# Performance work log

Measured on AMD Instinct MI355X. Metric: run time of the kernel, lower is better.

The kernel has to match this reference:

```python
import jax, jax.numpy as jnp
import numpy as np

ALPHA = 0.9  # init alpha, adj='DAD'


def setup_inputs() -> dict:
    key = jax.random.key(0)
    k1, k2, k3, k4 = jax.random.split(key, 4)
    N, C, E = 100000, 64, 3200000
    labels = jax.random.uniform(k1, (N, C), dtype=jnp.float32)
    mask = jax.random.randint(k2, (N,), 0, 2).astype(bool)
    src = jax.random.randint(k3, (E,), 0, N, dtype=jnp.int64)
    dst = jax.random.randint(k4, (E,), 0, N, dtype=jnp.int64)
    return {"labels": labels, "mask": mask, "src": src, "dst": dst, "num_layers": 10}


def reference(labels, mask, src, dst, num_layers):
    N = labels.shape[0]
    # mask: y = zeros; y[mask] = labels[mask]
    y0 = jnp.where(mask[:, None], labels, jnp.zeros((), labels.dtype))
    last = (1.0 - ALPHA) * y0  # confidence = 1
    # in-degrees via scatter-count at dst, clamped to >= 1
    degs = jax.ops.segment_sum(jnp.ones(dst.shape, labels.dtype), dst, num_segments=N)
    degs = jnp.maximum(degs, 1.0)
    norm = (degs ** -0.5)[:, None]  # DAD: D^-1/2 on both sides

    def step(y, _):
        y = norm * y                                   # left D^-1/2
        h = jax.ops.segment_sum(y[src], dst, num_segments=N)  # A @ y (copy_u + sum)
        y = ALPHA * h * norm                           # right D^-1/2
        y = jnp.clip(last + y, 0.0, 1.0)               # post_step clamp
        return y, None

    y, _ = jax.lax.scan(step, y0, None, length=num_layers)
    return y
```

## Files before the change

### kernel.cpp

```cpp
#include <hip/hip_runtime.h>
#include <hip/hip_fp16.h>


#define ALPHA 0.9f
#define C 64
#define BSHIFT 9
#define NCHUNK 256

typedef float f32x4 __attribute__((ext_vector_type(4)));
typedef unsigned int u32;


__global__ void chunk_hist_kernel(const int* __restrict__ dst, int* __restrict__ cnt,
                                  int E, int epc) {
    __shared__ int h[256];
    h[threadIdx.x] = 0;
    __syncthreads();
    int c = blockIdx.x;
    int e1 = min(c * epc + epc, E);
    for (int e = c * epc + threadIdx.x; e < e1; e += 256) {
        int d = __builtin_nontemporal_load(&dst[e]);
        atomicAdd(&h[d >> BSHIFT], 1);
    }
    __syncthreads();
    cnt[c * 256 + threadIdx.x] = h[threadIdx.x];
}

__global__ void bucket_scan_kernel(int* __restrict__ cnt, int* __restrict__ bucket_base,
                                   int* __restrict__ row_ptr, int N, int E) {
    __shared__ int tmp[256];
    int b = threadIdx.x;
    int s = 0;
    for (int c = 0; c < NCHUNK; ++c) {
        int t = cnt[c * 256 + b];
        cnt[c * 256 + b] = s;
        s += t;
    }
    tmp[b] = s;
    __syncthreads();
    int v = s;
    for (int off = 1; off < 256; off <<= 1) {
        int add = (b >= off) ? tmp[b - off] : 0;
        __syncthreads();
        tmp[b] += add;
        __syncthreads();
    }
    bucket_base[b] = tmp[b] - v;
    if (b == 255) { bucket_base[256] = tmp[255]; row_ptr[N] = E; }
}

__global__ void bucket_scatter_kernel(const int* __restrict__ src, const int* __restrict__ dst,
                                      const int* __restrict__ cnt,
                                      const int* __restrict__ bucket_base,
                                      unsigned* __restrict__ tmp, int E, int epc) {
    __shared__ int cur[256];
    int c = blockIdx.x;
    cur[threadIdx.x] = bucket_base[threadIdx.x] + cnt[c * 256 + threadIdx.x];
    __syncthreads();
    int e1 = min(c * epc + epc, E);
    for (int e = c * epc + threadIdx.x; e < e1; e += 256) {
        int d = __builtin_nontemporal_load(&dst[e]);
        int s = __builtin_nontemporal_load(&src[e]);
        int pos = atomicAdd(&cur[d >> BSHIFT], 1);
        tmp[pos] = ((unsigned)(d & 511) << 23) | (unsigned)s;
    }
}

__global__ void bucket_sort_kernel(const unsigned* __restrict__ tmp,
                                   const int* __restrict__ bucket_base,
                                   int* __restrict__ row_ptr,
                                   float* __restrict__ norm,
                                   int* __restrict__ col, int N) {
    __shared__ int ldeg[512];
    __shared__ int lexc[512];
    __shared__ int lcur[512];
    __shared__ int stmp[256];
    int b = blockIdx.x;
    int lo = b << BSHIFT;
    int nn = min(512, N - lo);
    int ebeg = bucket_base[b];
    int eend = bucket_base[b + 1];
    int t = threadIdx.x;
    ldeg[t] = 0; ldeg[t + 256] = 0;
    __syncthreads();
    for (int e = ebeg + t; e < eend; e += 256) {
        atomicAdd(&ldeg[tmp[e] >> 23], 1);
    }
    __syncthreads();
    int d0 = ldeg[2 * t], d1 = ldeg[2 * t + 1];
    int p = d0 + d1;
    stmp[t] = p;
    __syncthreads();
    for (int off = 1; off < 256; off <<= 1) {
        int add = (t >= off) ? stmp[t - off] : 0;
        __syncthreads();
        stmp[t] += add;
        __syncthreads();
    }
    int excp = stmp[t] - p;
    lexc[2 * t] = excp;
    lexc[2 * t + 1] = excp + d0;
    __syncthreads();
    for (int i = t; i < nn; i += 256) {
        int rp = ebeg + lexc[i];
        row_ptr[lo + i] = rp;
        lcur[i] = rp;
        norm[lo + i] = rsqrtf(fmaxf((float)ldeg[i], 1.0f));
    }
    __syncthreads();
    for (int e = ebeg + t; e < eend; e += 256) {
        unsigned pk = tmp[e];
        int pos = atomicAdd(&lcur[pk >> 23], 1);
        col[pos] = (int)(pk & 0x7FFFFFu);
    }
}

__global__ void pack_col_kernel(int* __restrict__ col, const float* __restrict__ norm,
                                int E) {
    int i = blockIdx.x * blockDim.x + threadIdx.x;
    if (i >= E) return;
    u32 s = (u32)col[i];
    u32 nq = (u32)(norm[s] * 32767.0f + 0.5f);
    col[i] = (int)(s | (nq << 17));
}


__global__ void init_z8_kernel(const float* __restrict__ labels,
                               const int* __restrict__ mask,
                               unsigned char* __restrict__ z8,
                               __half* __restrict__ last16,
                               int total8 ) {
    int i = blockIdx.x * blockDim.x + threadIdx.x;
    if (i >= total8) return;
    int node = i >> 3;
    int g = i & 7;
    const float* lrow = labels + (size_t)node * C + g * 8;
    f32x4 a  = __builtin_nontemporal_load((const f32x4*)lrow);
    f32x4 bv = __builtin_nontemporal_load((const f32x4*)lrow + 1);
    bool mk = mask[node] != 0;
    float v[8] = {a.x, a.y, a.z, a.w, bv.x, bv.y, bv.z, bv.w};
    float m = mk ? 255.0f : 0.0f;
    u32 q0 = 0, q1 = 0;
#pragma unroll
    for (int k = 0; k < 4; ++k) q0 |= ((u32)(v[k] * m + 0.5f)) << (8 * k);
#pragma unroll
    for (int k = 0; k < 4; ++k) q1 |= ((u32)(v[k + 4] * m + 0.5f)) << (8 * k);
    uint2 qq; qq.x = q0; qq.y = q1;
    ((uint2*)(z8 + (size_t)node * C))[g] = qq;
    if (last16) {
        float ml = mk ? (1.0f - ALPHA) : 0.0f;
        __half2 h[4];
        h[0] = __floats2half2_rn(ml * v[0], ml * v[1]);
        h[1] = __floats2half2_rn(ml * v[2], ml * v[3]);
        h[2] = __floats2half2_rn(ml * v[4], ml * v[5]);
        h[3] = __floats2half2_rn(ml * v[6], ml * v[7]);
        ((float4*)(last16 + (size_t)node * C))[g] = *(const float4*)h;
    }
}


template <bool OUT_FP32>
__global__ void prop_kernel(const unsigned char* __restrict__ z8_old,
                            unsigned char* __restrict__ z8_new,
                            void* __restrict__ out_f32,
                            const int* __restrict__ row_ptr,
                            const int* __restrict__ col,
                            const float* __restrict__ norm,
                            const __half* __restrict__ last16,
                            const float* __restrict__ labels,
                            const int* __restrict__ mask, int N) {
    int gtid = blockIdx.x * blockDim.x + threadIdx.x;
    int wid = gtid >> 6;
    int lane = threadIdx.x & 63;
    int node = (wid << 1) + (lane >> 5);
    int sub = (lane >> 3) & 3;
    int ch8 = lane & 7;

    bool ok = node < N;
    int beg = 0, end = 0;
    if (ok) { beg = row_ptr[node]; end = row_ptr[node + 1]; }
    int deg = end - beg;
    int lastc = max(end - 1, 0);
    int Tl = (deg + 3) >> 2;
    int T = max(Tl, __shfl_xor(Tl, 32, 64));

    const float DQ = 1.0f / (32767.0f * 255.0f);

    float acc[8];
#pragma unroll
    for (int k = 0; k < 8; ++k) acc[k] = 0.0f;

    if (T > 0) {
        int base = beg + sub;

        float n0, n1, n2, n3, n4, n5, n6, n7;
        uint2 r0, r1, r2, r3, r4, r5, r6, r7;

#define FETCH(t, nv, rv)                                                      \
        do {                                                                  \
            int pp = base + ((t) << 2);                                       \
            int pcl = min(pp, lastc);                                         \
            u32 pk = (u32)col[pcl];                                           \
            int sv = (int)(pk & 0x1FFFFu);                                    \
            float sc = (float)(pk >> 17) * DQ;                                \
            nv = (pp < end) ? sc : 0.0f;                                      \
            rv = ((const uint2*)(z8_old + (size_t)sv * C))[ch8];              \
        } while (0)

#define CONSUME(nv, rv)                                                       \
        do {                                                                  \
            u32 q0 = rv.x, q1 = rv.y;                                         \
            acc[0] = fmaf((float)(q0 & 0xffu),         nv, acc[0]);           \
            acc[1] = fmaf((float)((q0 >> 8) & 0xffu),  nv, acc[1]);           \
            acc[2] = fmaf((float)((q0 >> 16) & 0xffu), nv, acc[2]);           \
            acc[3] = fmaf((float)(q0 >> 24),           nv, acc[3]);           \
            acc[4] = fmaf((float)(q1 & 0xffu),         nv, acc[4]);           \
            acc[5] = fmaf((float)((q1 >> 8) & 0xffu),  nv, acc[5]);           \
            acc[6] = fmaf((float)((q1 >> 16) & 0xffu), nv, acc[6]);           \
            acc[7] = fmaf((float)(q1 >> 24),           nv, acc[7]);           \
        } while (0)

        FETCH(0, n0, r0); FETCH(1, n1, r1); FETCH(2, n2, r2); FETCH(3, n3, r3);
        FETCH(4, n4, r4); FETCH(5, n5, r5); FETCH(6, n6, r6); FETCH(7, n7, r7);
        int t = 8;
        for (; t + 8 <= T; t += 8) {
            CONSUME(n0, r0); FETCH(t + 0, n0, r0);
            CONSUME(n1, r1); FETCH(t + 1, n1, r1);
            CONSUME(n2, r2); FETCH(t + 2, n2, r2);
            CONSUME(n3, r3); FETCH(t + 3, n3, r3);
            CONSUME(n4, r4); FETCH(t + 4, n4, r4);
            CONSUME(n5, r5); FETCH(t + 5, n5, r5);
            CONSUME(n6, r6); FETCH(t + 6, n6, r6);
            CONSUME(n7, r7); FETCH(t + 7, n7, r7);
        }
        int rr = T - t;
        if (rr > 0) { CONSUME(n0, r0); FETCH(t + 0, n0, r0); }
        if (rr > 1) { CONSUME(n1, r1); FETCH(t + 1, n1, r1); }
        if (rr > 2) { CONSUME(n2, r2); FETCH(t + 2, n2, r2); }
        if (rr > 3) { CONSUME(n3, r3); FETCH(t + 3, n3, r3); }
        if (rr > 4) { CONSUME(n4, r4); FETCH(t + 4, n4, r4); }
        if (rr > 5) { CONSUME(n5, r5); FETCH(t + 5, n5, r5); }
        if (rr > 6) { CONSUME(n6, r6); FETCH(t + 6, n6, r6); }
        CONSUME(n0, r0); CONSUME(n1, r1); CONSUME(n2, r2); CONSUME(n3, r3);
        CONSUME(n4, r4); CONSUME(n5, r5); CONSUME(n6, r6); CONSUME(n7, r7);
#undef FETCH
#undef CONSUME
    }

#pragma unroll
    for (int k = 0; k < 8; ++k) {
        acc[k] += __shfl_xor(acc[k], 8, 64);
        acc[k] += __shfl_xor(acc[k], 16, 64);
    }

    if (sub == 0 && ok) {
        float nr = norm[node];
        float anr = ALPHA * nr;
        float la[8];
        if (last16) {
            float4 lv = ((const float4*)(last16 + (size_t)node * C))[ch8];
            const __half* lh = (const __half*)&lv;
#pragma unroll
            for (int k = 0; k < 8; ++k) la[k] = __half2float(lh[k]);
        } else {
            const float* lrow = labels + (size_t)node * C + ch8 * 8;
            float4 A = ((const float4*)lrow)[0];
            float4 Bv = ((const float4*)lrow)[1];
            float m = (mask[node] != 0) ? (1.0f - ALPHA) : 0.0f;
            la[0] = m * A.x;  la[1] = m * A.y;  la[2] = m * A.z;  la[3] = m * A.w;
            la[4] = m * Bv.x; la[5] = m * Bv.y; la[6] = m * Bv.z; la[7] = m * Bv.w;
        }
        float o[8];
#pragma unroll
        for (int k = 0; k < 8; ++k)
            o[k] = fminf(fmaxf(la[k] + anr * acc[k], 0.0f), 1.0f);
        if (OUT_FP32) {
            float* orow = (float*)out_f32 + (size_t)node * C + ch8 * 8;
            float4 v0; v0.x = o[0]; v0.y = o[1]; v0.z = o[2]; v0.w = o[3];
            float4 v1; v1.x = o[4]; v1.y = o[5]; v1.z = o[6]; v1.w = o[7];
            ((float4*)orow)[0] = v0;
            ((float4*)orow)[1] = v1;
        } else {
            u32 q0 = 0, q1 = 0;
#pragma unroll
            for (int k = 0; k < 4; ++k) q0 |= ((u32)(o[k] * 255.0f + 0.5f)) << (8 * k);
#pragma unroll
            for (int k = 0; k < 4; ++k) q1 |= ((u32)(o[k + 4] * 255.0f + 0.5f)) << (8 * k);
            uint2 qq; qq.x = q0; qq.y = q1;
            ((uint2*)(z8_new + (size_t)node * C))[ch8] = qq;
        }
    }
}


__global__ void zero_f32_kernel(float* __restrict__ p, int n) {
    int i = blockIdx.x * blockDim.x + threadIdx.x;
    if (i < n) p[i] = 0.0f;
}
__global__ void deg_count_f_kernel(const int* __restrict__ dst, float* __restrict__ deg, int E) {
    int i = blockIdx.x * blockDim.x + threadIdx.x;
    if (i < E) atomicAdd(&deg[dst[i]], 1.0f);
}
__global__ void make_norm_f_kernel(float* __restrict__ deg, int N) {
    int i = blockIdx.x * blockDim.x + threadIdx.x;
    if (i < N) deg[i] = rsqrtf(fmaxf(deg[i], 1.0f));
}
__global__ void init_yh_kernel(const float* __restrict__ labels, const int* __restrict__ mask,
                               float* __restrict__ y, float* __restrict__ h, int total4) {
    int i = blockIdx.x * blockDim.x + threadIdx.x;
    if (i >= total4) return;
    int row = i >> 4;
    float4 lv = ((const float4*)labels)[i];
    float m = (mask[row] != 0) ? 1.0f : 0.0f;
    float4 yv; yv.x = m * lv.x; yv.y = m * lv.y; yv.z = m * lv.z; yv.w = m * lv.w;
    ((float4*)y)[i] = yv;
    float4 z; z.x = 0.f; z.y = 0.f; z.z = 0.f; z.w = 0.f;
    ((float4*)h)[i] = z;
}
__global__ void scatter_kernel(const float* __restrict__ y, const int* __restrict__ src,
                               const int* __restrict__ dst, const float* __restrict__ norm,
                               float* __restrict__ h, int E) {
    int gtid = blockIdx.x * blockDim.x + threadIdx.x;
    int e = gtid >> 6;
    int lane = threadIdx.x & 63;
    if (e >= E) return;
    int s = src[e]; int d = dst[e];
    float v = y[(size_t)s * C + lane] * norm[s];
    atomicAdd(&h[(size_t)d * C + lane], v);
}
__global__ void finalize_kernel(const float* __restrict__ labels, const int* __restrict__ mask,
                                const float* __restrict__ norm, float* __restrict__ h,
                                float* __restrict__ y, int total4) {
    int i = blockIdx.x * blockDim.x + threadIdx.x;
    if (i >= total4) return;
    int row = i >> 4;
    float4 hv = ((float4*)h)[i];
    float4 lv = ((const float4*)labels)[i];
    float m = (mask[row] != 0) ? (1.0f - ALPHA) : 0.0f;
    float nr = norm[row];
    float4 o;
    o.x = fminf(fmaxf(m * lv.x + ALPHA * hv.x * nr, 0.0f), 1.0f);
    o.y = fminf(fmaxf(m * lv.y + ALPHA * hv.y * nr, 0.0f), 1.0f);
    o.z = fminf(fmaxf(m * lv.z + ALPHA * hv.z * nr, 0.0f), 1.0f);
    o.w = fminf(fmaxf(m * lv.w + ALPHA * hv.w * nr, 0.0f), 1.0f);
    ((float4*)y)[i] = o;
    float4 z; z.x = 0.f; z.y = 0.f; z.z = 0.f; z.w = 0.f;
    ((float4*)h)[i] = z;
}


extern "C" void kernel_launch(void* const* d_in, const int* in_sizes, int n_in,
                              void* d_out, int out_size, void* d_ws, size_t ws_size,
                              hipStream_t stream) {
    const float* labels = (const float*)d_in[0];
    const int*   mask   = (const int*)d_in[1];
    const int*   src    = (const int*)d_in[2];
    const int*   dst    = (const int*)d_in[3];

    const int N = in_sizes[1];
    const int E = in_sizes[2];
    const int num_layers = 10;
    const int B = 256;

    size_t fixed_ints = (size_t)257 + (size_t)NCHUNK * 256 + (N + 1) + N + E;
    size_t z8bytes = (size_t)N * C;
    size_t tmpbytes = (size_t)E * 4;
    size_t span = (tmpbytes > 2 * z8bytes ? tmpbytes : 2 * z8bytes);
    size_t l16bytes = (size_t)N * C * 2;
    size_t need_base = fixed_ints * 4 + 256 + span;
    size_t need_l16  = need_base + l16bytes;
    bool pack_ok = (N < (1 << 17));

    if (ws_size >= need_base && pack_ok) {
        char* w = (char*)d_ws;
        int*   bucket_base = (int*)w;             w += 257 * 4;
        int*   cnt         = (int*)w;             w += (size_t)NCHUNK * 256 * 4;
        int*   row_ptr     = (int*)w;             w += (size_t)(N + 1) * 4;
        float* norm        = (float*)w;           w += (size_t)N * 4;
        int*   col         = (int*)w;             w += (size_t)E * 4;
        w = (char*)(((uintptr_t)w + 255) & ~(uintptr_t)255);
        unsigned char* z8A = (unsigned char*)w;
        unsigned char* z8B = z8A + z8bytes;
        unsigned* tmp      = (unsigned*)z8A;
        w += span;
        __half* last16     = (ws_size >= need_l16) ? (__half*)w : nullptr;

        int epc = (E + NCHUNK - 1) / NCHUNK;
        int NB = (N + 511) >> BSHIFT;

        chunk_hist_kernel<<<NCHUNK, 256, 0, stream>>>(dst, cnt, E, epc);
        bucket_scan_kernel<<<1, 256, 0, stream>>>(cnt, bucket_base, row_ptr, N, E);
        bucket_scatter_kernel<<<NCHUNK, 256, 0, stream>>>(src, dst, cnt, bucket_base,
                                                          tmp, E, epc);
        bucket_sort_kernel<<<NB, 256, 0, stream>>>(tmp, bucket_base, row_ptr,
                                                   norm, col, N);
        pack_col_kernel<<<(E + B - 1) / B, B, 0, stream>>>(col, norm, E);

        int total8 = N * 8;
        init_z8_kernel<<<(total8 + B - 1) / B, B, 0, stream>>>(labels, mask,
                                                               z8A, last16, total8);
        const int nwaves = (N + 1) >> 1;
        const int prop_blocks = (int)(((size_t)nwaves * 64 + B - 1) / B);
        for (int l = 0; l < num_layers - 1; ++l) {
            unsigned char* zi = (l & 1) ? z8B : z8A;
            unsigned char* zo = (l & 1) ? z8A : z8B;
            prop_kernel<false><<<prop_blocks, B, 0, stream>>>(zi, zo, nullptr,
                                                              row_ptr, col, norm,
                                                              last16, labels, mask, N);
        }
        prop_kernel<true><<<prop_blocks, B, 0, stream>>>(z8B, nullptr, d_out,
                                                         row_ptr, col, norm,
                                                         last16, labels, mask, N);
    } else {
        const int total4 = N * C / 4;
        float* y = (float*)d_out;
        float* wsf = (float*)d_ws;
        float* norm = wsf;
        float* h = wsf + ((N + 15) & ~15);
        zero_f32_kernel<<<(N + B - 1) / B, B, 0, stream>>>(norm, N);
        deg_count_f_kernel<<<(E + B - 1) / B, B, 0, stream>>>(dst, norm, E);
        make_norm_f_kernel<<<(N + B - 1) / B, B, 0, stream>>>(norm, N);
        init_yh_kernel<<<(total4 + B - 1) / B, B, 0, stream>>>(labels, mask, y, h, total4);
        const int scatter_blocks = (int)(((size_t)E * C + B - 1) / B);
        for (int l = 0; l < num_layers; ++l) {
            scatter_kernel<<<scatter_blocks, B, 0, stream>>>(y, src, dst, norm, h, E);
            finalize_kernel<<<(total4 + B - 1) / B, B, 0, stream>>>(labels, mask, norm,
                                                                    h, y, total4);
        }
    }
}
```

Baseline: 661.2 us.

## Fuse norm packing into bucket sort, precompute degrees, store last term as uint8

Degree norms are now computed up front with float atomics on dst, so bucket_sort can pack the quantized source norm into col directly. That removes the separate pack_col pass over all edges. The (1-alpha)*y0 residual term is stored as 8-bit, reusing the already quantized z8 values, instead of fp16, which halves its per-layer read traffic in prop_kernel. The cost is an extra atomic-heavy degree pass over E edges, plus coarser precision for the residual term.

```diff
diff --git a/kernel.cpp b/kernel.cpp
--- a/kernel.cpp
+++ b/kernel.cpp
@@ -9,6 +9,21 @@
 
 typedef float f32x4 __attribute__((ext_vector_type(4)));
 typedef unsigned int u32;
+typedef unsigned int u32x2 __attribute__((ext_vector_type(2)));
+
+
+__global__ void zero_f32_kernel(float* __restrict__ p, int n) {
+    int i = blockIdx.x * blockDim.x + threadIdx.x;
+    if (i < n) p[i] = 0.0f;
+}
+__global__ void deg_count_f_kernel(const int* __restrict__ dst, float* __restrict__ deg, int E) {
+    int i = blockIdx.x * blockDim.x + threadIdx.x;
+    if (i < E) atomicAdd(&deg[__builtin_nontemporal_load(&dst[i])], 1.0f);
+}
+__global__ void make_norm_f_kernel(float* __restrict__ deg, int N) {
+    int i = blockIdx.x * blockDim.x + threadIdx.x;
+    if (i < N) deg[i] = rsqrtf(fmaxf(deg[i], 1.0f));
+}
 
 
 __global__ void chunk_hist_kernel(const int* __restrict__ dst, int* __restrict__ cnt,
@@ -69,7 +84,7 @@
 __global__ void bucket_sort_kernel(const unsigned* __restrict__ tmp,
                                    const int* __restrict__ bucket_base,
                                    int* __restrict__ row_ptr,
-                                   float* __restrict__ norm,
+                                   const float* __restrict__ norm,
                                    int* __restrict__ col, int N) {
     __shared__ int ldeg[512];
     __shared__ int lexc[512];
@@ -105,30 +120,22 @@
         int rp = ebeg + lexc[i];
         row_ptr[lo + i] = rp;
         lcur[i] = rp;
-        norm[lo + i] = rsqrtf(fmaxf((float)ldeg[i], 1.0f));
     }
     __syncthreads();
     for (int e = ebeg + t; e < eend; e += 256) {
         unsigned pk = tmp[e];
         int pos = atomicAdd(&lcur[pk >> 23], 1);
-        col[pos] = (int)(pk & 0x7FFFFFu);
-    }
-}
-
-__global__ void pack_col_kernel(int* __restrict__ col, const float* __restrict__ norm,
-                                int E) {
-    int i = blockIdx.x * blockDim.x + threadIdx.x;
-    if (i >= E) return;
-    u32 s = (u32)col[i];
-    u32 nq = (u32)(norm[s] * 32767.0f + 0.5f);
-    col[i] = (int)(s | (nq << 17));
+        u32 s = pk & 0x7FFFFFu;
+        u32 nq = (u32)(norm[s] * 32767.0f + 0.5f);
+        col[pos] = (int)(s | (nq << 17));
+    }
 }
 
 
 __global__ void init_z8_kernel(const float* __restrict__ labels,
                                const int* __restrict__ mask,
                                unsigned char* __restrict__ z8,
-                               __half* __restrict__ last16,
+                               unsigned char* __restrict__ last8,
                                int total8 ) {
     int i = blockIdx.x * blockDim.x + threadIdx.x;
     if (i >= total8) return;
@@ -145,17 +152,9 @@
     for (int k = 0; k < 4; ++k) q0 |= ((u32)(v[k] * m + 0.5f)) << (8 * k);
 #pragma unroll
     for (int k = 0; k < 4; ++k) q1 |= ((u32)(v[k + 4] * m + 0.5f)) << (8 * k);
-    uint2 qq; qq.x = q0; qq.y = q1;
-    ((uint2*)(z8 + (size_t)node * C))[g] = qq;
-    if (last16) {
-        float ml = mk ? (1.0f - ALPHA) : 0.0f;
-        __half2 h[4];
-        h[0] = __floats2half2_rn(ml * v[0], ml * v[1]);
-        h[1] = __floats2half2_rn(ml * v[2], ml * v[3]);
-        h[2] = __floats2half2_rn(ml * v[4], ml * v[5]);
-        h[3] = __floats2half2_rn(ml * v[6], ml * v[7]);
-        ((float4*)(last16 + (size_t)node * C))[g] = *(const float4*)h;
-    }
+    u32x2 qq; qq.x = q0; qq.y = q1;
+    ((u32x2*)(z8 + (size_t)node * C))[g] = qq;
+    ((u32x2*)(last8 + (size_t)node * C))[g] = qq;
 }
 
 
@@ -166,9 +165,7 @@
                             const int* __restrict__ row_ptr,
                             const int* __restrict__ col,
                             const float* __restrict__ norm,
-                            const __half* __restrict__ last16,
-                            const float* __restrict__ labels,
-                            const int* __restrict__ mask, int N) {
+                            const unsigned char* __restrict__ last8, int N) {
     int gtid = blockIdx.x * blockDim.x + threadIdx.x;
     int wid = gtid >> 6;
     int lane = threadIdx.x & 63;
@@ -256,24 +253,23 @@
     if (sub == 0 && ok) {
         float nr = norm[node];
         float anr = ALPHA * nr;
+        const float LC = (1.0f - ALPHA) / 255.0f;
+        u32x2 lq = __builtin_nontemporal_load(
+            (const u32x2*)(last8 + (size_t)node * C) + ch8);
+        u32 l0 = lq.x, l1 = lq.y;
         float la[8];
-        if (last16) {
-            float4 lv = ((const float4*)(last16 + (size_t)node * C))[ch8];
-            const __half* lh = (const __half*)&lv;
-#pragma unroll
-            for (int k = 0; k < 8; ++k) la[k] = __half2float(lh[k]);
-        } else {
-            const float* lrow = labels + (size_t)node * C + ch8 * 8;
-            float4 A = ((const float4*)lrow)[0];
-            float4 Bv = ((const float4*)lrow)[1];
-            float m = (mask[node] != 0) ? (1.0f - ALPHA) : 0.0f;
-            la[0] = m * A.x;  la[1] = m * A.y;  la[2] = m * A.z;  la[3] = m * A.w;
-            la[4] = m * Bv.x; la[5] = m * Bv.y; la[6] = m * Bv.z; la[7] = m * Bv.w;
-        }
+        la[0] = (float)(l0 & 0xffu) * LC;
+        la[1] = (float)((l0 >> 8) & 0xffu) * LC;
+        la[2] = (float)((l0 >> 16) & 0xffu) * LC;
+        la[3] = (float)(l0 >> 24) * LC;
+        la[4] = (float)(l1 & 0xffu) * LC;
+        la[5] = (float)((l1 >> 8) & 0xffu) * LC;
+        la[6] = (float)((l1 >> 16) & 0xffu) * LC;
+        la[7] = (float)(l1 >> 24) * LC;
         float o[8];
 #pragma unroll
         for (int k = 0; k < 8; ++k)
-            o[k] = fminf(fmaxf(la[k] + anr * acc[k], 0.0f), 1.0f);
+            o[k] = fminf(fmaxf(fmaf(anr, acc[k], la[k]), 0.0f), 1.0f);
         if (OUT_FP32) {
             float* orow = (float*)out_f32 + (size_t)node * C + ch8 * 8;
             float4 v0; v0.x = o[0]; v0.y = o[1]; v0.z = o[2]; v0.w = o[3];
@@ -293,18 +289,6 @@
 }
 
 
-__global__ void zero_f32_kernel(float* __restrict__ p, int n) {
-    int i = blockIdx.x * blockDim.x + threadIdx.x;
-    if (i < n) p[i] = 0.0f;
-}
-__global__ void deg_count_f_kernel(const int* __restrict__ dst, float* __restrict__ deg, int E) {
-    int i = blockIdx.x * blockDim.x + threadIdx.x;
-    if (i < E) atomicAdd(&deg[dst[i]], 1.0f);
-}
-__global__ void make_norm_f_kernel(float* __restrict__ deg, int N) {
-    int i = blockIdx.x * blockDim.x + threadIdx.x;
-    if (i < N) deg[i] = rsqrtf(fmaxf(deg[i], 1.0f));
-}
 __global__ void init_yh_kernel(const float* __restrict__ labels, const int* __restrict__ mask,
                                float* __restrict__ y, float* __restrict__ h, int total4) {
     int i = blockIdx.x * blockDim.x + threadIdx.x;
@@ -366,12 +350,10 @@
     size_t z8bytes = (size_t)N * C;
     size_t tmpbytes = (size_t)E * 4;
     size_t span = (tmpbytes > 2 * z8bytes ? tmpbytes : 2 * z8bytes);
-    size_t l16bytes = (size_t)N * C * 2;
-    size_t need_base = fixed_ints * 4 + 256 + span;
-    size_t need_l16  = need_base + l16bytes;
+    size_t need = fixed_ints * 4 + 256 + span + z8bytes;
     bool pack_ok = (N < (1 << 17));
 
-    if (ws_size >= need_base && pack_ok) {
+    if (ws_size >= need && pack_ok) {
         char* w = (char*)d_ws;
         int*   bucket_base = (int*)w;             w += 257 * 4;
         int*   cnt         = (int*)w;             w += (size_t)NCHUNK * 256 * 4;
@@ -383,10 +365,14 @@
         unsigned char* z8B = z8A + z8bytes;
         unsigned* tmp      = (unsigned*)z8A;
         w += span;
-        __half* last16     = (ws_size >= need_l16) ? (__half*)w : nullptr;
+        unsigned char* last8 = (unsigned char*)w;
 
         int epc = (E + NCHUNK - 1) / NCHUNK;
         int NB = (N + 511) >> BSHIFT;
+
+        zero_f32_kernel<<<(N + B - 1) / B, B, 0, stream>>>(norm, N);
+        deg_count_f_kernel<<<(E + B - 1) / B, B, 0, stream>>>(dst, norm, E);
+        make_norm_f_kernel<<<(N + B - 1) / B, B, 0, stream>>>(norm, N);
 
         chunk_hist_kernel<<<NCHUNK, 256, 0, stream>>>(dst, cnt, E, epc);
         bucket_scan_kernel<<<1, 256, 0, stream>>>(cnt, bucket_base, row_ptr, N, E);
@@ -394,11 +380,10 @@
                                                           tmp, E, epc);
         bucket_sort_kernel<<<NB, 256, 0, stream>>>(tmp, bucket_base, row_ptr,
                                                    norm, col, N);
-        pack_col_kernel<<<(E + B - 1) / B, B, 0, stream>>>(col, norm, E);
 
         int total8 = N * 8;
         init_z8_kernel<<<(total8 + B - 1) / B, B, 0, stream>>>(labels, mask,
-                                                               z8A, last16, total8);
+                                                               z8A, last8, total8);
         const int nwaves = (N + 1) >> 1;
         const int prop_blocks = (int)(((size_t)nwaves * 64 + B - 1) / B);
         for (int l = 0; l < num_layers - 1; ++l) {
@@ -406,11 +391,11 @@
             unsigned char* zo = (l & 1) ? z8A : z8B;
             prop_kernel<false><<<prop_blocks, B, 0, stream>>>(zi, zo, nullptr,
                                                               row_ptr, col, norm,
-                                                              last16, labels, mask, N);
+                                                              last8, N);
         }
         prop_kernel<true><<<prop_blocks, B, 0, stream>>>(z8B, nullptr, d_out,
                                                          row_ptr, col, norm,
-                                                         last16, labels, mask, N);
+                                                         last8, N);
     } else {
         const int total4 = N * C / 4;
         float* y = (float*)d_out;
```

Result: slower. 846.8 us (+28.1%).
